# Performance work log

Hardware: AMD Instinct MI355X
Metric: run time of the kernel (lower is better)

Reference implementation:

```python
import jax, jax.numpy as jnp
import numpy as np

EPS = 1e-5

def _conv(x, w):
    # x: [B,C,H,W], w: [K,C,3,3] -> [B,K,H,W]; stacks all centroid convs into one conv
    return jax.lax.conv_general_dilated(
        x, w, window_strides=(1, 1), padding=((1, 1), (1, 1)),
        dimension_numbers=("NCHW", "OIHW", "NCHW"))

def _bn(x, gamma, beta, mean, var):
    # inference-mode BatchNorm2d over channel axis 1
    inv = gamma / jnp.sqrt(var + EPS)
    return x * inv[None, :, None, None] + (beta - mean * inv)[None, :, None, None]

def setup_inputs() -> dict:
    key = jax.random.key(0)
    ks = jax.random.split(key, 16)
    B, C, H, W, K = 32, 256, 56, 56, 16
    d = {}
    d["x"] = jax.random.normal(ks[0], (B, C, H, W), jnp.float32)
    d["w1"] = jax.random.normal(ks[1], (K, C, 3, 3), jnp.float32) * 0.05
    d["b1"] = jax.random.normal(ks[2], (K,), jnp.float32) * 0.05
    d["w2"] = jax.random.normal(ks[3], (K, C, 3, 3), jnp.float32) * 0.05
    d["b2"] = jax.random.normal(ks[4], (K,), jnp.float32) * 0.05
    d["gamma1"] = jax.random.uniform(ks[5], (C,), jnp.float32)
    d["beta1"] = jax.random.normal(ks[6], (C,), jnp.float32) * 0.1
    d["mean1"] = jax.random.normal(ks[7], (C,), jnp.float32) * 0.1
    d["var1"] = jax.random.uniform(ks[8], (C,), jnp.float32)
    d["gamma2"] = jax.random.uniform(ks[9], (C,), jnp.float32)
    d["beta2"] = jax.random.normal(ks[10], (C,), jnp.float32) * 0.1
    d["mean2"] = jax.random.normal(ks[11], (C,), jnp.float32) * 0.1
    d["var2"] = jax.random.uniform(ks[12], (C,), jnp.float32)
    d["labels1"] = jax.random.randint(ks[13], (C,), 0, K, jnp.int64)
    d["labels2"] = jax.random.randint(ks[14], (C,), 0, K, jnp.int64)
    return d

def reference(x, w1, b1, w2, b2, gamma1, beta1, mean1, var1,
              gamma2, beta2, mean2, var2, labels1, labels2):
    # centroids_apply: run all K centroid convs at once, then label-indexed
    # channel gather (equivalent to the original per-centroid conv + concat)
    y1 = _conv(x, w1)[:, labels1] + b1[labels1][None, :, None, None]
    h = jax.nn.relu(_bn(y1, gamma1, beta1, mean1, var1))
    y2 = _conv(h, w2)[:, labels2] + b2[labels2][None, :, None, None]
    out = _bn(y2, gamma2, beta2, mean2, var2) + x  # identity residual (no skipper)
    return jax.nn.relu(out)
```

## Files before the change

### kernel.cpp

```cpp
#include <hip/hip_runtime.h>
#include <cstddef>
#include <cstdint>

typedef short short8 __attribute__((ext_vector_type(8)));
typedef float f32x4 __attribute__((ext_vector_type(4)));

namespace {
constexpr int B = 32, C = 256, H = 56, W = 56, K = 16;
constexpr int HW = H * W;
constexpr int WP = 58, PP = 58 * 58;
constexpr float EPS = 1e-5f;

constexpr size_t OFF_WF1 = 0;
constexpr size_t OFF_WF2 = 73728;
constexpr size_t OFF_A1 = 147456, OFF_D1 = 148480;
constexpr size_t OFF_A2 = 149504, OFF_D2 = 150528;
constexpr size_t OFF_G1 = 151552, OFF_G2 = 152576;
constexpr size_t OFF_XT = 153600;
constexpr size_t XT_BYTES = (size_t)B * PP * C * 2;
constexpr size_t OFF_Z1 = OFF_XT + XT_BYTES;
constexpr size_t OFF_Z2 = OFF_Z1 + (size_t)B * HW * 16 * 4;
constexpr int BORDER_U4 = 32 * 228 * 32;
}

__device__ inline ushort f2bf(float f) {
  uint32_t u = __float_as_uint(f);
  u += 0x7fff + ((u >> 16) & 1);
  return (ushort)(u >> 16);
}

__global__ __launch_bounds__(256) void prep_kernel(
    const float* __restrict__ w1, const float* __restrict__ b1,
    const float* __restrict__ w2, const float* __restrict__ b2,
    const float* __restrict__ gamma1, const float* __restrict__ beta1,
    const float* __restrict__ mean1, const float* __restrict__ var1,
    const float* __restrict__ gamma2, const float* __restrict__ beta2,
    const float* __restrict__ mean2, const float* __restrict__ var2,
    const int* __restrict__ lab1, const int* __restrict__ lab2,
    char* __restrict__ wsb) {
  int bid = blockIdx.x, tid = threadIdx.x;
  if (bid < 288) {
    int i = bid * 256 + tid;
    int which = i >= 36864;
    int ii = which ? i - 36864 : i;
    int j = ii & 7, lane = (ii >> 3) & 63, cc = (ii >> 9) & 7, t = ii >> 12;
    int c = cc * 32 + ((lane >> 4) << 3) + j;
    int k = lane & 15;
    const float* w = which ? w2 : w1;
    ushort* wf = (ushort*)(wsb + (which ? OFF_WF2 : OFF_WF1));
    wf[ii] = f2bf(w[k * (C * 9) + c * 9 + t]);
    if (i < C) {
      int g1 = lab1[i], g2 = lab2[i];
      float a1 = gamma1[i] / sqrtf(var1[i] + EPS);
      float a2 = gamma2[i] / sqrtf(var2[i] + EPS);
      ((float*)(wsb + OFF_A1))[i] = a1;
      ((float*)(wsb + OFF_D1))[i] = a1 * b1[g1] + beta1[i] - mean1[i] * a1;
      ((float*)(wsb + OFF_A2))[i] = a2;
      ((float*)(wsb + OFF_D2))[i] = a2 * b2[g2] + beta2[i] - mean2[i] * a2;
      ((int*)(wsb + OFF_G1))[i] = g1;
      ((int*)(wsb + OFF_G2))[i] = g2;
    }
  } else {
    int idx = (bid - 288) * 256 + tid;
    if (idx < BORDER_U4) {
      int pix = idx >> 5, q = idx & 31;
      int b = pix / 228, e = pix - b * 228;
      int y, x;
      if (e < 58) { y = 0; x = e; }
      else if (e < 116) { y = 57; x = e - 58; }
      else if (e < 172) { y = e - 115; x = 0; }
      else { y = e - 171; x = 57; }
      size_t off = OFF_XT + ((size_t)b * PP + y * WP + x) * 512 + (size_t)q * 16;
      int4 z = {0, 0, 0, 0};
      *(int4*)(wsb + off) = z;
    }
  }
}

__global__ __launch_bounds__(256) void transpose_kernel(
    const float* __restrict__ x, char* __restrict__ wsb) {
  __shared__ float t[64][65];
  int bid = blockIdx.x;
  int b = bid / 196, rem = bid - b * 196, pt = rem >> 2, ct = rem & 3;
  int p0 = pt * 64, c0 = ct * 64;
  int tid = threadIdx.x, lane = tid & 63, grp = tid >> 6;
  const float* xb = x + ((size_t)b * C + c0) * HW + p0;
#pragma unroll
  for (int r = 0; r < 16; ++r) {
    int row = r * 4 + grp;
    t[row][lane] = xb[(size_t)row * HW + lane];
  }
  __syncthreads();
  ushort* xt = (ushort*)(wsb + OFF_XT) + (size_t)b * PP * C;
  int c2 = (tid & 31) * 2, g = tid >> 5;
#pragma unroll
  for (int r = 0; r < 8; ++r) {
    int prow = r * 8 + g;
    int p = p0 + prow;
    int y = p / 56, xx = p - y * 56;
    uint v = (uint)f2bf(t[c2][prow]) | ((uint)f2bf(t[c2 + 1][prow]) << 16);
    *(uint*)(xt + ((size_t)(y + 1) * WP + xx + 1) * C + c0 + c2) = v;
  }
}

__global__ __launch_bounds__(256, 2) void conv1_kernel(char* __restrict__ wsb) {
  __shared__ char sbuf[59392];
  const int tid = threadIdx.x, lane = tid & 63, wave = tid >> 6;
  const int row = lane & 15, blk = lane >> 4;
  int bid = blockIdx.x;
  int wg = (bid & 7) * 112 + (bid >> 3);
  int b = wg / 28, j = wg - b * 28;
  int y0 = 2 * j;
  const char* xtb = wsb + OFF_XT + (size_t)b * (PP * C * 2);
  const char* wf = wsb + OFF_WF1;

  int addrA[2][9][2];
#pragma unroll
  for (int f = 0; f < 2; ++f) {
    int fr = (f == 1) ? (wave + 4) : wave;
    if (fr > 6) fr = wave;
    int op = fr * 16 + row;
    int oy = (op >= 56) ? 1 : 0;
    int pib = (oy + 1) * 58 + (op - oy * 56) + 1;
#pragma unroll
    for (int t = 0; t < 9; ++t) {
      int pi = pib + (t / 3 - 1) * 58 + (t % 3 - 1);
      int swz = (pi & 7) << 4;
      addrA[f][t][0] = pi * 128 + ((blk * 16) ^ swz);
      addrA[f][t][1] = pi * 128 + ((64 + blk * 16) ^ swz);
    }
  }
  f32x4 acc0 = {0.f, 0.f, 0.f, 0.f}, acc1 = {0.f, 0.f, 0.f, 0.f};

  auto fill = [&](int cc, char* buf) {
#pragma unroll
    for (int i = 0; i < 8; ++i) {
      int idx = i * 256 + tid;
      if (idx < 1856) {
        int pi = idx >> 3, sub = idx & 7;
        int r = pi / 58, xx = pi - r * 58;
        const char* src =
            xtb + (((size_t)(y0 + r) * 58 + xx) * 256 + cc * 64) * 2 + sub * 16;
        int4 v = *(const int4*)src;
        *(int4*)(buf + pi * 128 + ((sub * 16) ^ ((pi & 7) << 4))) = v;
      }
    }
  };
  auto mstep = [&](int cc, const char* buf) {
#pragma unroll
    for (int t = 0; t < 9; ++t) {
#pragma unroll
      for (int ks = 0; ks < 2; ++ks) {
        short8 bf =
            *(const short8*)(wf + ((t * 8 + cc * 2 + ks) * 64 + lane) * 16);
        short8 a0 = *(const short8*)(buf + addrA[0][t][ks]);
        acc0 = __builtin_amdgcn_mfma_f32_16x16x32_bf16(a0, bf, acc0, 0, 0, 0);
        if (wave < 3) {
          short8 a1 = *(const short8*)(buf + addrA[1][t][ks]);
          acc1 = __builtin_amdgcn_mfma_f32_16x16x32_bf16(a1, bf, acc1, 0, 0, 0);
        }
      }
    }
  };

  fill(0, sbuf);
  __syncthreads();
  for (int cc = 0; cc < 4; ++cc) {
    if (cc < 3) fill(cc + 1, sbuf + ((cc + 1) & 1) * 29696);
    mstep(cc, sbuf + (cc & 1) * 29696);
    __syncthreads();
  }
  float* zs = (float*)sbuf;
#pragma unroll
  for (int i = 0; i < 4; ++i) {
    zs[(wave * 16 + blk * 4 + i) * 17 + row] = acc0[i];
    if (wave < 3) zs[((wave + 4) * 16 + blk * 4 + i) * 17 + row] = acc1[i];
  }
  __syncthreads();
  float* z1 = (float*)(wsb + OFF_Z1) + ((size_t)b * HW + y0 * 56) * 16;
#pragma unroll
  for (int i = 0; i < 2; ++i) {
    int id = i * 256 + tid;
    if (id < 448) {
      int px = id >> 2, q = id & 3;
      f32x4 v;
      v.x = zs[px * 17 + q * 4 + 0];
      v.y = zs[px * 17 + q * 4 + 1];
      v.z = zs[px * 17 + q * 4 + 2];
      v.w = zs[px * 17 + q * 4 + 3];
      *(f32x4*)(z1 + (size_t)id * 4) = v;
    }
  }
}

__global__ __launch_bounds__(256, 2) void conv2_kernel(char* __restrict__ wsb) {
  __shared__ char sbuf[75168];
  const int tid = threadIdx.x, lane = tid & 63, wave = tid >> 6;
  const int row = lane & 15, blk = lane >> 4;
  int bid = blockIdx.x;
  int wg = (bid & 7) * 112 + (bid >> 3);
  int b = wg / 28, j = wg - b * 28;
  int y0 = 2 * j;
  const char* wf = wsb + OFF_WF2;
  float* zt = (float*)(sbuf + 59392);

#pragma unroll
  for (int i = 0; i < 16; ++i) {
    int id = i * 256 + tid;
    if (id < 3944) zt[id] = 0.f;
  }
  __syncthreads();
  const float* z1 = (const float*)(wsb + OFF_Z1) + (size_t)b * HW * 16;
#pragma unroll
  for (int i = 0; i < 4; ++i) {
    int id = i * 256 + tid;
    if (id < 896) {
      int r = id / 224, rem = id - r * 224, xx = rem >> 2, q = rem & 3;
      int yg = y0 - 1 + r;
      if (yg >= 0 && yg < 56) {
        f32x4 v = *(const f32x4*)(z1 + ((size_t)yg * 56 + xx) * 16 + q * 4);
        int base = (r * 58 + xx + 1) * 17 + q * 4;
        zt[base + 0] = v.x;
        zt[base + 1] = v.y;
        zt[base + 2] = v.z;
        zt[base + 3] = v.w;
      }
    }
  }

  int addrA[2][9][2];
#pragma unroll
  for (int f = 0; f < 2; ++f) {
    int fr = (f == 1) ? (wave + 4) : wave;
    if (fr > 6) fr = wave;
    int op = fr * 16 + row;
    int oy = (op >= 56) ? 1 : 0;
    int pib = (oy + 1) * 58 + (op - oy * 56) + 1;
#pragma unroll
    for (int t = 0; t < 9; ++t) {
      int pi = pib + (t / 3 - 1) * 58 + (t % 3 - 1);
      int swz = (pi & 7) << 4;
      addrA[f][t][0] = pi * 128 + ((blk * 16) ^ swz);
      addrA[f][t][1] = pi * 128 + ((64 + blk * 16) ^ swz);
    }
  }
  f32x4 acc0 = {0.f, 0.f, 0.f, 0.f}, acc1 = {0.f, 0.f, 0.f, 0.f};
  const int cp = tid & 31, pig = tid >> 5;
  const float* A1 = (const float*)(wsb + OFF_A1);
  const float* D1 = (const float*)(wsb + OFF_D1);
  const int* G1 = (const int*)(wsb + OFF_G1);

  auto expand = [&](int cc, char* buf) {
    int c = cc * 64 + cp * 2;
    float2 a = *(const float2*)(A1 + c);
    float2 dd = *(const float2*)(D1 + c);
    int2 g = *(const int2*)(G1 + c);
#pragma unroll 4
    for (int i = 0; i < 29; ++i) {
      int pi = pig + i * 8;
      float za = zt[pi * 17 + g.x], zb = zt[pi * 17 + g.y];
      float h0 = fmaxf(fmaf(a.x, za, dd.x), 0.f);
      float h1 = fmaxf(fmaf(a.y, zb, dd.y), 0.f);
      uint u = (uint)f2bf(h0) | ((uint)f2bf(h1) << 16);
      *(uint*)(buf + pi * 128 + ((cp * 4) ^ ((pi & 7) << 4))) = u;
    }
  };
  auto mstep = [&](int cc, const char* buf) {
#pragma unroll
    for (int t = 0; t < 9; ++t) {
#pragma unroll
      for (int ks = 0; ks < 2; ++ks) {
        short8 bf =
            *(const short8*)(wf + ((t * 8 + cc * 2 + ks) * 64 + lane) * 16);
        short8 a0 = *(const short8*)(buf + addrA[0][t][ks]);
        acc0 = __builtin_amdgcn_mfma_f32_16x16x32_bf16(a0, bf, acc0, 0, 0, 0);
        if (wave < 3) {
          short8 a1 = *(const short8*)(buf + addrA[1][t][ks]);
          acc1 = __builtin_amdgcn_mfma_f32_16x16x32_bf16(a1, bf, acc1, 0, 0, 0);
        }
      }
    }
  };

  __syncthreads();
  expand(0, sbuf);
  __syncthreads();
  for (int cc = 0; cc < 4; ++cc) {
    if (cc < 3) expand(cc + 1, sbuf + ((cc + 1) & 1) * 29696);
    mstep(cc, sbuf + (cc & 1) * 29696);
    __syncthreads();
  }
  float* zs = (float*)sbuf;
#pragma unroll
  for (int i = 0; i < 4; ++i) {
    zs[(wave * 16 + blk * 4 + i) * 17 + row] = acc0[i];
    if (wave < 3) zs[((wave + 4) * 16 + blk * 4 + i) * 17 + row] = acc1[i];
  }
  __syncthreads();
  float* z2 = (float*)(wsb + OFF_Z2) + ((size_t)b * HW + y0 * 56) * 16;
#pragma unroll
  for (int i = 0; i < 2; ++i) {
    int id = i * 256 + tid;
    if (id < 448) {
      int px = id >> 2, q = id & 3;
      f32x4 v;
      v.x = zs[px * 17 + q * 4 + 0];
      v.y = zs[px * 17 + q * 4 + 1];
      v.z = zs[px * 17 + q * 4 + 2];
      v.w = zs[px * 17 + q * 4 + 3];
      *(f32x4*)(z2 + (size_t)id * 4) = v;
    }
  }
}

__global__ __launch_bounds__(256) void epilogue_kernel(
    const float* __restrict__ x, const char* __restrict__ wsb,
    float* __restrict__ out) {
  int bid = blockIdx.x;
  int wg = (bid & 7) * 112 + (bid >> 3);
  int b = wg / 28, j = wg - b * 28;
  int p0 = 2 * j * 56;
  int tid = threadIdx.x;
  int q = tid & 31, cg = tid >> 5;
  bool act = q < 28;
  const float* A2 = (const float*)(wsb + OFF_A2);
  const float* D2 = (const float*)(wsb + OFF_D2);
  const int* G2 = (const int*)(wsb + OFF_G2);
  const float* z2 = (const float*)(wsb + OFF_Z2) + ((size_t)b * HW + p0) * 16;
  size_t xb = (size_t)b * C * HW + p0 + q * 4;
#pragma unroll 4
  for (int i = 0; i < 32; ++i) {
    int c = i * 8 + cg;
    if (act) {
      float a = A2[c], d = D2[c];
      int g = G2[c];
      const float* zr = z2 + q * 64 + g;
      f32x4 xv = *(const f32x4*)(x + xb + (size_t)c * HW);
      f32x4 v;
      v.x = fmaxf(fmaf(a, zr[0], d) + xv.x, 0.f);
      v.y = fmaxf(fmaf(a, zr[16], d) + xv.y, 0.f);
      v.z = fmaxf(fmaf(a, zr[32], d) + xv.z, 0.f);
      v.w = fmaxf(fmaf(a, zr[48], d) + xv.w, 0.f);
      *(f32x4*)(out + xb + (size_t)c * HW) = v;
    }
  }
}

extern "C" void kernel_launch(void* const* d_in, const int* in_sizes, int n_in,
                              void* d_out, int out_size, void* d_ws,
                              size_t ws_size, hipStream_t stream) {
  const float* x = (const float*)d_in[0];
  const float* w1 = (const float*)d_in[1];
  const float* b1 = (const float*)d_in[2];
  const float* w2 = (const float*)d_in[3];
  const float* b2 = (const float*)d_in[4];
  const float* gamma1 = (const float*)d_in[5];
  const float* beta1 = (const float*)d_in[6];
  const float* mean1 = (const float*)d_in[7];
  const float* var1 = (const float*)d_in[8];
  const float* gamma2 = (const float*)d_in[9];
  const float* beta2 = (const float*)d_in[10];
  const float* mean2 = (const float*)d_in[11];
  const float* var2 = (const float*)d_in[12];
  const int* lab1 = (const int*)d_in[13];
  const int* lab2 = (const int*)d_in[14];
  char* wsb = (char*)d_ws;
  float* out = (float*)d_out;

  prep_kernel<<<288 + 912, 256, 0, stream>>>(
      w1, b1, w2, b2, gamma1, beta1, mean1, var1, gamma2, beta2, mean2, var2,
      lab1, lab2, wsb);
  transpose_kernel<<<32 * 196, 256, 0, stream>>>(x, wsb);
  conv1_kernel<<<896, 256, 0, stream>>>(wsb);
  conv2_kernel<<<896, 256, 0, stream>>>(wsb);
  epilogue_kernel<<<896, 256, 0, stream>>>(x, wsb, out);
}
```

Measured before the change: 363.5 us.

## Switch MFMA to fp16 and store conv2 output planar for flat epilogue

Replaces bf16 conversion and bf16 MFMA with fp16 conversion and fp16 MFMA across the weights, the transposed input and the intermediate activations, which mainly changes precision rather than throughput. Conv2 now writes its 16-channel result in a planar [B,16,HW] layout, so the epilogue becomes a flat elementwise kernel with one float4 per thread and a vector load of the gathered centroid plane. This is meant to improve coalescing of the z2 reads, which were strided scalar loads before, at the cost of more blocks. fp16 carries a risk of overflow or precision differences compared with bf16.

```diff
diff --git a/kernel.cpp b/kernel.cpp
--- a/kernel.cpp
+++ b/kernel.cpp
@@ -2,7 +2,7 @@
 #include <cstddef>
 #include <cstdint>
 
-typedef short short8 __attribute__((ext_vector_type(8)));
+typedef _Float16 half8 __attribute__((ext_vector_type(8)));
 typedef float f32x4 __attribute__((ext_vector_type(4)));
 
 namespace {
@@ -23,10 +23,9 @@
 constexpr int BORDER_U4 = 32 * 228 * 32;
 }
 
-__device__ inline ushort f2bf(float f) {
-  uint32_t u = __float_as_uint(f);
-  u += 0x7fff + ((u >> 16) & 1);
-  return (ushort)(u >> 16);
+__device__ inline ushort f2h(float f) {
+  _Float16 h = (_Float16)f;
+  return __builtin_bit_cast(ushort, h);
 }
 
 __global__ __launch_bounds__(256) void prep_kernel(
@@ -48,7 +47,7 @@
     int k = lane & 15;
     const float* w = which ? w2 : w1;
     ushort* wf = (ushort*)(wsb + (which ? OFF_WF2 : OFF_WF1));
-    wf[ii] = f2bf(w[k * (C * 9) + c * 9 + t]);
+    wf[ii] = f2h(w[k * (C * 9) + c * 9 + t]);
     if (i < C) {
       int g1 = lab1[i], g2 = lab2[i];
       float a1 = gamma1[i] / sqrtf(var1[i] + EPS);
@@ -98,7 +97,7 @@
     int prow = r * 8 + g;
     int p = p0 + prow;
     int y = p / 56, xx = p - y * 56;
-    uint v = (uint)f2bf(t[c2][prow]) | ((uint)f2bf(t[c2 + 1][prow]) << 16);
+    uint v = (uint)f2h(t[c2][prow]) | ((uint)f2h(t[c2 + 1][prow]) << 16);
     *(uint*)(xt + ((size_t)(y + 1) * WP + xx + 1) * C + c0 + c2) = v;
   }
 }
@@ -151,13 +150,13 @@
     for (int t = 0; t < 9; ++t) {
 #pragma unroll
       for (int ks = 0; ks < 2; ++ks) {
-        short8 bf =
-            *(const short8*)(wf + ((t * 8 + cc * 2 + ks) * 64 + lane) * 16);
-        short8 a0 = *(const short8*)(buf + addrA[0][t][ks]);
-        acc0 = __builtin_amdgcn_mfma_f32_16x16x32_bf16(a0, bf, acc0, 0, 0, 0);
+        half8 bf =
+            *(const half8*)(wf + ((t * 8 + cc * 2 + ks) * 64 + lane) * 16);
+        half8 a0 = *(const half8*)(buf + addrA[0][t][ks]);
+        acc0 = __builtin_amdgcn_mfma_f32_16x16x32_f16(a0, bf, acc0, 0, 0, 0);
         if (wave < 3) {
-          short8 a1 = *(const short8*)(buf + addrA[1][t][ks]);
-          acc1 = __builtin_amdgcn_mfma_f32_16x16x32_bf16(a1, bf, acc1, 0, 0, 0);
+          half8 a1 = *(const half8*)(buf + addrA[1][t][ks]);
+          acc1 = __builtin_amdgcn_mfma_f32_16x16x32_f16(a1, bf, acc1, 0, 0, 0);
         }
       }
     }
@@ -261,7 +260,7 @@
       float za = zt[pi * 17 + g.x], zb = zt[pi * 17 + g.y];
       float h0 = fmaxf(fmaf(a.x, za, dd.x), 0.f);
       float h1 = fmaxf(fmaf(a.y, zb, dd.y), 0.f);
-      uint u = (uint)f2bf(h0) | ((uint)f2bf(h1) << 16);
+      uint u = (uint)f2h(h0) | ((uint)f2h(h1) << 16);
       *(uint*)(buf + pi * 128 + ((cp * 4) ^ ((pi & 7) << 4))) = u;
     }
   };
@@ -270,13 +269,13 @@
     for (int t = 0; t < 9; ++t) {
 #pragma unroll
       for (int ks = 0; ks < 2; ++ks) {
-        short8 bf =
-            *(const short8*)(wf + ((t * 8 + cc * 2 + ks) * 64 + lane) * 16);
-        short8 a0 = *(const short8*)(buf + addrA[0][t][ks]);
-        acc0 = __builtin_amdgcn_mfma_f32_16x16x32_bf16(a0, bf, acc0, 0, 0, 0);
+        half8 bf =
+            *(const half8*)(wf + ((t * 8 + cc * 2 + ks) * 64 + lane) * 16);
+        half8 a0 = *(const half8*)(buf + addrA[0][t][ks]);
+        acc0 = __builtin_amdgcn_mfma_f32_16x16x32_f16(a0, bf, acc0, 0, 0, 0);
         if (wave < 3) {
-          short8 a1 = *(const short8*)(buf + addrA[1][t][ks]);
-          acc1 = __builtin_amdgcn_mfma_f32_16x16x32_bf16(a1, bf, acc1, 0, 0, 0);
+          half8 a1 = *(const half8*)(buf + addrA[1][t][ks]);
+          acc1 = __builtin_amdgcn_mfma_f32_16x16x32_f16(a1, bf, acc1, 0, 0, 0);
         }
       }
     }
@@ -297,18 +296,18 @@
     if (wave < 3) zs[((wave + 4) * 16 + blk * 4 + i) * 17 + row] = acc1[i];
   }
   __syncthreads();
-  float* z2 = (float*)(wsb + OFF_Z2) + ((size_t)b * HW + y0 * 56) * 16;
+  float* z2 = (float*)(wsb + OFF_Z2);
 #pragma unroll
   for (int i = 0; i < 2; ++i) {
     int id = i * 256 + tid;
     if (id < 448) {
-      int px = id >> 2, q = id & 3;
+      int k = id / 28, q = id - k * 28;
       f32x4 v;
-      v.x = zs[px * 17 + q * 4 + 0];
-      v.y = zs[px * 17 + q * 4 + 1];
-      v.z = zs[px * 17 + q * 4 + 2];
-      v.w = zs[px * 17 + q * 4 + 3];
-      *(f32x4*)(z2 + (size_t)id * 4) = v;
+      v.x = zs[(q * 4 + 0) * 17 + k];
+      v.y = zs[(q * 4 + 1) * 17 + k];
+      v.z = zs[(q * 4 + 2) * 17 + k];
+      v.w = zs[(q * 4 + 3) * 17 + k];
+      *(f32x4*)(z2 + ((size_t)(b * 16 + k) * HW + y0 * 56 + q * 4)) = v;
     }
   }
 }
@@ -316,34 +315,23 @@
 __global__ __launch_bounds__(256) void epilogue_kernel(
     const float* __restrict__ x, const char* __restrict__ wsb,
     float* __restrict__ out) {
-  int bid = blockIdx.x;
-  int wg = (bid & 7) * 112 + (bid >> 3);
-  int b = wg / 28, j = wg - b * 28;
-  int p0 = 2 * j * 56;
-  int tid = threadIdx.x;
-  int q = tid & 31, cg = tid >> 5;
-  bool act = q < 28;
-  const float* A2 = (const float*)(wsb + OFF_A2);
-  const float* D2 = (const float*)(wsb + OFF_D2);
-  const int* G2 = (const int*)(wsb + OFF_G2);
-  const float* z2 = (const float*)(wsb + OFF_Z2) + ((size_t)b * HW + p0) * 16;
-  size_t xb = (size_t)b * C * HW + p0 + q * 4;
-#pragma unroll 4
-  for (int i = 0; i < 32; ++i) {
-    int c = i * 8 + cg;
-    if (act) {
-      float a = A2[c], d = D2[c];
-      int g = G2[c];
-      const float* zr = z2 + q * 64 + g;
-      f32x4 xv = *(const f32x4*)(x + xb + (size_t)c * HW);
-      f32x4 v;
-      v.x = fmaxf(fmaf(a, zr[0], d) + xv.x, 0.f);
-      v.y = fmaxf(fmaf(a, zr[16], d) + xv.y, 0.f);
-      v.z = fmaxf(fmaf(a, zr[32], d) + xv.z, 0.f);
-      v.w = fmaxf(fmaf(a, zr[48], d) + xv.w, 0.f);
-      *(f32x4*)(out + xb + (size_t)c * HW) = v;
-    }
-  }
+  int idx = blockIdx.x * 256 + threadIdx.x;
+  int p4 = idx % 784;
+  int t = idx / 784;
+  int c = t & 255, b = t >> 8;
+  float a = ((const float*)(wsb + OFF_A2))[c];
+  float d = ((const float*)(wsb + OFF_D2))[c];
+  int g = ((const int*)(wsb + OFF_G2))[c];
+  const float* zp =
+      (const float*)(wsb + OFF_Z2) + ((size_t)(b * 16 + g) * HW + p4 * 4);
+  f32x4 z = *(const f32x4*)zp;
+  f32x4 xv = *(const f32x4*)(x + (size_t)idx * 4);
+  f32x4 v;
+  v.x = fmaxf(fmaf(a, z.x, d) + xv.x, 0.f);
+  v.y = fmaxf(fmaf(a, z.y, d) + xv.y, 0.f);
+  v.z = fmaxf(fmaf(a, z.z, d) + xv.z, 0.f);
+  v.w = fmaxf(fmaf(a, z.w, d) + xv.w, 0.f);
+  *(f32x4*)(out + (size_t)idx * 4) = v;
 }
 
 extern "C" void kernel_launch(void* const* d_in, const int* in_sizes, int n_in,
@@ -373,5 +361,5 @@
   transpose_kernel<<<32 * 196, 256, 0, stream>>>(x, wsb);
   conv1_kernel<<<896, 256, 0, stream>>>(wsb);
   conv2_kernel<<<896, 256, 0, stream>>>(wsb);
-  epilogue_kernel<<<896, 256, 0, stream>>>(x, wsb, out);
-}
+  epilogue_kernel<<<25088, 256, 0, stream>>>(x, wsb, out);
+}
```

Result: faster. 327.9 us (-9.8%).
